# Kernel tuning notes

Hardware: AMD Instinct MI355X
Metric: run time of the kernel (lower is better)

The kernel has to match this reference:

```python
import jax, jax.numpy as jnp
import numpy as np

# Module config (init_kwargs): shape_data=(5,32,32), pow=1, diff_only=False
N_T, N_Y, N_X = 5, 32, 32
N = N_Y * N_X          # nb_nodes = 1024
N_B = 2                # batch
DX = DY = DT = 1.0


def softplus_b(x, beta):
    # torch F.softplus(x, beta) = (1/beta) * log(1 + exp(beta*x))
    return jax.nn.softplus(beta * x) / beta


def build_A(kappa, m, H):
    """Dense finite-difference SPDE operator A = kappa^2 I + m.grad - div(H grad).
    kappa: (N,), m: (2,N), H: (2,2,N). Returns (N,N).
    (DiffOperator source is not in the provided snippet; this is the standard
    4dvarnet SPDE 9-point stencil discretization with dx=dy=1.)"""
    idx = jnp.arange(N)
    xx = idx % N_X
    yy = idx // N_X
    H11, H22 = H[0, 0], H[1, 1]
    H12 = 0.5 * (H[0, 1] + H[1, 0])
    m1, m2 = m[0], m[1]
    center = kappa ** 2 + 2.0 * H11 + 2.0 * H22
    A = jnp.zeros((N, N), dtype=kappa.dtype).at[idx, idx].set(center)
    stencil = [
        ( 1,  0, -H11 + 0.5 * m1),
        (-1,  0, -H11 - 0.5 * m1),
        ( 0,  1, -H22 + 0.5 * m2),
        ( 0, -1, -H22 - 0.5 * m2),
        ( 1,  1, -0.5 * H12),
        (-1, -1, -0.5 * H12),
        ( 1, -1,  0.5 * H12),
        (-1,  1,  0.5 * H12),
    ]
    for dxo, dyo, c in stencil:
        nx_, ny_ = xx + dxo, yy + dyo
        valid = (nx_ >= 0) & (nx_ < N_X) & (ny_ >= 0) & (ny_ < N_Y)
        nbr = jnp.clip(ny_, 0, N_Y - 1) * N_X + jnp.clip(nx_, 0, N_X - 1)
        A = A.at[idx, nbr].add(jnp.where(valid, c, 0.0))
    return A


def decode_params(params):
    """Faithful decode_param_CNN.forward (including its raw-reshape axis mixing)."""
    nb = params.shape[0]
    kappa = softplus_b(params[:, :N_T], 10.0)
    kappa = kappa.reshape(nb, 1, N, N_T)                     # raw reshape as in torch
    m = jnp.stack([params[:, N_T:2 * N_T], params[:, 2 * N_T:3 * N_T]], axis=1)
    m = m.reshape(nb, 2, N, N_T)                             # raw reshape as in torch
    gamma = softplus_b(params[:, 3 * N_T:4 * N_T], 10.0)
    gamma = gamma.transpose(0, 2, 3, 1).reshape(nb, N * N_T)  # (y,x,t) order
    vx = params[:, 4 * N_T:5 * N_T].transpose(0, 2, 3, 1).reshape(nb, N * N_T)
    vy = params[:, 5 * N_T:6 * N_T].transpose(0, 2, 3, 1).reshape(nb, N * N_T)
    vxy = jnp.stack([vx, vy], axis=2)                        # (b, K, 2)
    # H[b,i,j,k] = gamma[b,k]*delta_ij + v_i[b,k]*v_j[b,k]
    H = (jnp.eye(2, dtype=params.dtype)[None, :, :, None] * gamma[:, None, None, :]
         + jnp.einsum('bki,bkj->bijk', vxy, vxy))
    H = H.reshape(nb, 2, 2, N, N_T)
    return kappa, m, H


def reference(params):
    """Prior_SPDE.forward(decode_param_CNN(params), square_root=False) -> dense Q.
    Note: in create_Q (diff_only=False) tau is overwritten with ones and
    QR/Q0 are reassigned to Id / B0^T B0, so tau channels are dead code."""
    kappa, m, H = decode_params(params)
    # operators built for time indices k+1, k=0..n_t-2
    kap_t = jnp.moveaxis(kappa[:, 0, :, 1:], -1, 1).reshape(N_B * (N_T - 1), N)
    m_t = jnp.moveaxis(m[:, :, :, 1:], -1, 1).reshape(N_B * (N_T - 1), 2, N)
    H_t = jnp.moveaxis(H[:, :, :, :, 1:], -1, 1).reshape(N_B * (N_T - 1), 2, 2, N)
    A = jax.vmap(build_A)(kap_t, m_t, H_t).reshape(N_B, N_T - 1, N, N)
    I = jnp.eye(N, dtype=params.dtype)
    invM = A * DT + I                      # Id + dt*B, B = A (pow=1)
    M2 = jnp.matmul(invM, invM)            # inv_M[i]^2
    B0 = A[:, 0]
    Q = jnp.zeros((N_B, N_T * N, N_T * N), dtype=params.dtype)
    s = lambda i: slice(i * N, (i + 1) * N)
    # row 0: [B0^T B0 + I, -inv_M[0], 0...]
    Q = Q.at[:, s(0), s(0)].set(jnp.einsum('bki,bkj->bij', B0, B0) + I)
    Q = Q.at[:, s(0), s(1)].set(-invM[:, 0])
    # rows 1..n_t-2: [..., -inv_M[i-1], inv_M[i-1]^2 + I, -inv_M[i], ...]
    for i in range(1, N_T - 1):
        Q = Q.at[:, s(i), s(i - 1)].set(-invM[:, i - 1])
        Q = Q.at[:, s(i), s(i)].set(M2[:, i - 1] + I)
        Q = Q.at[:, s(i), s(i + 1)].set(-invM[:, i])
    # last row: [..., -inv_M[n_t-2], inv_M[n_t-2]^2]
    Q = Q.at[:, s(N_T - 1), s(N_T - 2)].set(-invM[:, N_T - 2])
    Q = Q.at[:, s(N_T - 1), s(N_T - 1)].set(M2[:, N_T - 2])
    Q = 0.5 * (Q + jnp.swapaxes(Q, 1, 2)) + 0.05 * jnp.eye(N_T * N, dtype=params.dtype)
    return Q


def setup_inputs() -> dict:
    key = jax.random.key(0)
    params = jax.random.normal(key, (N_B, 7 * N_T, N_Y, N_X), dtype=jnp.float32)
    return {"params": params}
```

## Files before the change

kernel.cpp:

```cpp
#include <hip/hip_runtime.h>


#define AC_OFF   0
#define OFFD_OFF 73728
#define DIAG_OFF 147456

__device__ __forceinline__ float softplus10(float x) {
  float z = 10.f * x;
  return (fmaxf(z, 0.f) + log1pf(expf(-fabsf(z)))) * 0.1f;
}

__global__ __launch_bounds__(256) void decode_kernel(
    const float* __restrict__ P0, float* __restrict__ Ac) {
  int gid = blockIdx.x * 256 + threadIdx.x;
  if (gid >= 8 * 1024) return;
  int i = gid >> 10;
  int p = gid & 1023;
  int b = i >> 2;
  int t = (i & 3) + 1;
  const float* P = P0 + b * 35 * 1024;

  int qq = p * 5 + t;
  int c  = qq >> 10;
  int r  = qq & 1023;
  float kap = softplus10(P[(0 + c) * 1024 + r]);
  float m1  = P[(5 + c) * 1024 + r];
  float m2  = P[(10 + c) * 1024 + r];

  float g  = softplus10(P[(15 + t) * 1024 + p]);
  float vx = P[(20 + t) * 1024 + p];
  float vy = P[(25 + t) * 1024 + p];

  float H11 = g + vx * vx;
  float H22 = g + vy * vy;
  float H12 = vx * vy;

  float co[9];
  co[4] = kap * kap + 2.f * H11 + 2.f * H22;
  co[5] = -H11 + 0.5f * m1;
  co[3] = -H11 - 0.5f * m1;
  co[7] = -H22 + 0.5f * m2;
  co[1] = -H22 - 0.5f * m2;
  co[8] = -0.5f * H12;
  co[0] = -0.5f * H12;
  co[2] =  0.5f * H12;
  co[6] =  0.5f * H12;

  int px = p & 31, py = p >> 5;
  #pragma unroll
  for (int o = 0; o < 9; o++) {
    const int dx = o % 3 - 1, dy = o / 3 - 1;
    int nx = px + dx, ny = py + dy;
    bool valid = (nx >= 0) & (nx < 32) & (ny >= 0) & (ny < 32);
    Ac[(i * 1024 + p) * 9 + o] = (o == 4) ? co[4] : (valid ? co[o] : 0.f);
  }
}

__device__ __forceinline__ float m2e(const float* __restrict__ Ac, int i, int p, int q) {
  int px = p & 31, py = p >> 5, qx = q & 31, qy = q >> 5;
  float s = 0.f;
  #pragma unroll
  for (int o = 0; o < 9; o++) {
    const int dx = o % 3 - 1, dy = o / 3 - 1;
    int kx = px + dx, ky = py + dy;
    if (kx < 0 || kx > 31 || ky < 0 || ky > 31) continue;
    int k = ky * 32 + kx;
    float a = Ac[(i * 1024 + p) * 9 + o] + (o == 4 ? 1.f : 0.f);
    int ddx = qx - kx, ddy = qy - ky;
    if (ddx < -1 || ddx > 1 || ddy < -1 || ddy > 1) continue;
    float bb = Ac[(i * 1024 + k) * 9 + (ddy + 1) * 3 + (ddx + 1)] + (k == q ? 1.f : 0.f);
    s += a * bb;
  }
  return s;
}

__device__ __forceinline__ float btb(const float* __restrict__ Ac, int i0, int p, int q) {
  int px = p & 31, py = p >> 5, qx = q & 31, qy = q >> 5;
  float s = 0.f;
  #pragma unroll
  for (int o = 0; o < 9; o++) {
    const int dx = o % 3 - 1, dy = o / 3 - 1;
    int kx = px + dx, ky = py + dy;
    if (kx < 0 || kx > 31 || ky < 0 || ky > 31) continue;
    int k = ky * 32 + kx;
    float bkp = Ac[(i0 * 1024 + k) * 9 + (8 - o)];
    int ddx = qx - kx, ddy = qy - ky;
    if (ddx < -1 || ddx > 1 || ddy < -1 || ddy > 1) continue;
    float bkq = Ac[(i0 * 1024 + k) * 9 + (ddy + 1) * 3 + (ddx + 1)];
    s += bkp * bkq;
  }
  return s;
}

__global__ __launch_bounds__(256) void tables_kernel(float* __restrict__ ws) {
  const float* Ac = ws + AC_OFF;
  int gid = blockIdx.x * 256 + threadIdx.x;
  if (gid < 73728) {
    int i = gid / 9216;
    int rem = gid - i * 9216;
    int p = rem / 9;
    int o = rem - p * 9;
    int px = p & 31, py = p >> 5;
    int dx = o % 3 - 1, dy = o / 3 - 1;
    float v = 0.f;
    if (o == 4) {
      v = -(Ac[(i * 1024 + p) * 9 + 4] + 1.f);
    } else {
      int nx = px + dx, ny = py + dy;
      if (nx >= 0 && nx < 32 && ny >= 0 && ny < 32) {
        int q = ny * 32 + nx;
        v = -0.5f * (Ac[(i * 1024 + p) * 9 + o] + Ac[(i * 1024 + q) * 9 + (8 - o)]);
      }
    }
    ws[OFFD_OFF + gid] = v;
  } else {
    int e = gid - 73728;
    if (e >= 256000) return;
    int j = e / 25600;
    int rem = e - j * 25600;
    int p = rem / 25;
    int w = rem - p * 25;
    int b = j / 5, rb = j - b * 5;
    int px = p & 31, py = p >> 5;
    int dx = w % 5 - 2, dy = w / 5 - 2;
    int nx = px + dx, ny = py + dy;
    float v = 0.f;
    if (nx >= 0 && nx < 32 && ny >= 0 && ny < 32) {
      int q = ny * 32 + nx;
      if (rb == 0) {
        v = btb(Ac, b * 4, p, q) + (p == q ? 1.05f : 0.f);
      } else {
        int i = b * 4 + rb - 1;
        float diagAdd = (rb <= 3 ? 1.05f : 0.05f);
        v = 0.5f * (m2e(Ac, i, p, q) + m2e(Ac, i, q, p)) + (p == q ? diagAdd : 0.f);
      }
    }
    ws[DIAG_OFF + e] = v;
  }
}

__global__ __launch_bounds__(256) void fill_kernel(
    const float* __restrict__ ws, float4* __restrict__ out) {
  const int cb  = blockIdx.x;
  const int row = blockIdx.y;
  const int b   = blockIdx.z;
  const int tx  = threadIdx.x;
  const int rb  = row >> 10;
  const int p   = row & 1023;
  const int d   = cb - rb;
  const long oidx = (long)b * 6553600 + (long)row * 1280 + cb * 256 + tx;

  float4 v = make_float4(0.f, 0.f, 0.f, 0.f);
  if (d >= -1 && d <= 1) {
    const int q0  = tx * 4;
    const int qy  = q0 >> 5;
    const int qx0 = q0 & 31;
    const int px  = p & 31, py = p >> 5;
    const int dy  = qy - py;
    float rr[4] = {0.f, 0.f, 0.f, 0.f};
    if (d != 0) {
      if (dy >= -1 && dy <= 1) {
        const int i = b * 4 + (d > 0 ? rb : cb);
        const float* t = ws + OFFD_OFF + ((i * 1024 + p) * 9 + (dy + 1) * 3 + 1) - px;
        #pragma unroll
        for (int jj = 0; jj < 4; jj++) {
          int dx = qx0 + jj - px;
          if (dx >= -1 && dx <= 1) rr[jj] = t[qx0 + jj];
        }
      }
    } else {
      if (dy >= -2 && dy <= 2) {
        const int j = b * 5 + rb;
        const float* t = ws + DIAG_OFF + ((j * 1024 + p) * 25 + (dy + 2) * 5 + 2) - px;
        #pragma unroll
        for (int jj = 0; jj < 4; jj++) {
          int dx = qx0 + jj - px;
          if (dx >= -2 && dx <= 2) rr[jj] = t[qx0 + jj];
        }
      }
    }
    v = make_float4(rr[0], rr[1], rr[2], rr[3]);
  }
  out[oidx] = v;
}

extern "C" void kernel_launch(void* const* d_in, const int* in_sizes, int n_in,
                              void* d_out, int out_size, void* d_ws, size_t ws_size,
                              hipStream_t stream) {
  const float* params = (const float*)d_in[0];
  float* ws = (float*)d_ws;
  float4* out = (float4*)d_out;

  decode_kernel<<<32, 256, 0, stream>>>(params, ws + AC_OFF);
  tables_kernel<<<1288, 256, 0, stream>>>(ws);
  dim3 grid(5, 5120, 2);
  fill_kernel<<<grid, 256, 0, stream>>>(ws, out);
}
```

Before: 208.9 us.

## Split dense fill into nontemporal zero pass plus sparse band scatter

Replaces the fill kernel, which computed every float4 of the 210 MB output with banded branching, with two kernels. A grid-stride zero kernel writes the whole matrix using nontemporal vector stores, and a band kernel then scatters only the nonzero stencil entries (25 diagonal-block and 9 off-diagonal-block values per row). The aim is a pure streaming write for the bulk of the output. In exchange it adds a launch, scattered scalar writes, and an ordering dependency between the two passes on the same stream.

Measured after the change: 236.9 us. 1.13x slower.

```diff
diff --git a/kernel.cpp b/kernel.cpp
--- a/kernel.cpp
+++ b/kernel.cpp
@@ -4,6 +4,8 @@
 #define AC_OFF   0
 #define OFFD_OFF 73728
 #define DIAG_OFF 147456
+
+typedef float vfloat4 __attribute__((ext_vector_type(4)));
 
 __device__ __forceinline__ float softplus10(float x) {
   float z = 10.f * x;
@@ -139,49 +141,55 @@
   }
 }
 
-__global__ __launch_bounds__(256) void fill_kernel(
-    const float* __restrict__ ws, float4* __restrict__ out) {
-  const int cb  = blockIdx.x;
-  const int row = blockIdx.y;
-  const int b   = blockIdx.z;
-  const int tx  = threadIdx.x;
+__global__ __launch_bounds__(256) void zero_kernel(float* __restrict__ out) {
+  const long n4 = 13107200;
+  long idx = (long)blockIdx.x * 256 + threadIdx.x;
+  const long stride = (long)gridDim.x * 256;
+  vfloat4* o4 = (vfloat4*)out;
+  const vfloat4 z = (vfloat4)(0.f);
+  for (; idx < n4; idx += stride) {
+    __builtin_nontemporal_store(z, &o4[idx]);
+  }
+}
+
+__global__ __launch_bounds__(256) void band_kernel(
+    const float* __restrict__ ws, float* __restrict__ out) {
+  const int row = blockIdx.x * 4 + (threadIdx.x >> 6);
+  const int b   = blockIdx.y;
+  const int t   = threadIdx.x & 63;
   const int rb  = row >> 10;
   const int p   = row & 1023;
-  const int d   = cb - rb;
-  const long oidx = (long)b * 6553600 + (long)row * 1280 + cb * 256 + tx;
-
-  float4 v = make_float4(0.f, 0.f, 0.f, 0.f);
-  if (d >= -1 && d <= 1) {
-    const int q0  = tx * 4;
-    const int qy  = q0 >> 5;
-    const int qx0 = q0 & 31;
-    const int px  = p & 31, py = p >> 5;
-    const int dy  = qy - py;
-    float rr[4] = {0.f, 0.f, 0.f, 0.f};
-    if (d != 0) {
-      if (dy >= -1 && dy <= 1) {
-        const int i = b * 4 + (d > 0 ? rb : cb);
-        const float* t = ws + OFFD_OFF + ((i * 1024 + p) * 9 + (dy + 1) * 3 + 1) - px;
-        #pragma unroll
-        for (int jj = 0; jj < 4; jj++) {
-          int dx = qx0 + jj - px;
-          if (dx >= -1 && dx <= 1) rr[jj] = t[qx0 + jj];
-        }
-      }
-    } else {
-      if (dy >= -2 && dy <= 2) {
-        const int j = b * 5 + rb;
-        const float* t = ws + DIAG_OFF + ((j * 1024 + p) * 25 + (dy + 2) * 5 + 2) - px;
-        #pragma unroll
-        for (int jj = 0; jj < 4; jj++) {
-          int dx = qx0 + jj - px;
-          if (dx >= -2 && dx <= 2) rr[jj] = t[qx0 + jj];
-        }
-      }
-    }
-    v = make_float4(rr[0], rr[1], rr[2], rr[3]);
-  }
-  out[oidx] = v;
+  const int px  = p & 31, py = p >> 5;
+
+  int cb, dx, dy;
+  float v;
+  if (t < 25) {
+    cb = rb;
+    dx = t % 5 - 2;
+    dy = t / 5 - 2;
+    v = ws[DIAG_OFF + ((b * 5 + rb) * 1024 + p) * 25 + t];
+  } else if (t < 34) {
+    if (rb == 0) return;
+    cb = rb - 1;
+    const int o = t - 25;
+    dx = o % 3 - 1;
+    dy = o / 3 - 1;
+    v = ws[OFFD_OFF + ((b * 4 + rb - 1) * 1024 + p) * 9 + o];
+  } else if (t < 43) {
+    if (rb == 4) return;
+    cb = rb + 1;
+    const int o = t - 34;
+    dx = o % 3 - 1;
+    dy = o / 3 - 1;
+    v = ws[OFFD_OFF + ((b * 4 + rb) * 1024 + p) * 9 + o];
+  } else {
+    return;
+  }
+
+  const int nx = px + dx, ny = py + dy;
+  if (nx < 0 || nx > 31 || ny < 0 || ny > 31) return;
+  const int q = ny * 32 + nx;
+  out[(long)b * 26214400 + (long)row * 5120 + cb * 1024 + q] = v;
 }
 
 extern "C" void kernel_launch(void* const* d_in, const int* in_sizes, int n_in,
@@ -189,10 +197,11 @@
                               hipStream_t stream) {
   const float* params = (const float*)d_in[0];
   float* ws = (float*)d_ws;
-  float4* out = (float4*)d_out;
+  float* out = (float*)d_out;
 
   decode_kernel<<<32, 256, 0, stream>>>(params, ws + AC_OFF);
   tables_kernel<<<1288, 256, 0, stream>>>(ws);
-  dim3 grid(5, 5120, 2);
-  fill_kernel<<<grid, 256, 0, stream>>>(ws, out);
-}
+  zero_kernel<<<6400, 256, 0, stream>>>(out);
+  dim3 bgrid(1280, 2);
+  band_kernel<<<bgrid, 256, 0, stream>>>(ws, out);
+}
```

## Fuse decode into table kernel via LDS and write full rows per block

Applied to the files above, without the earlier changes.

Folds the stencil-coefficient decode into the table-building kernel. Each block recomputes the 1024-node coefficient set into shared memory and builds its slice of the off-diagonal and diagonal stencil tables from LDS, which removes one launch and the global round trip for the coefficients. The fill kernel now has one block per output row that writes all five column blocks, so each block loads its stencil values once instead of once per column block. In exchange the decode work is repeated across 16 slices per table, and the fused kernel runs on only 160 blocks.

Measured after the change: 215.7 us. 1.03x slower.

```diff
diff --git a/kernel.cpp b/kernel.cpp
--- a/kernel.cpp
+++ b/kernel.cpp
@@ -1,62 +1,17 @@
 #include <hip/hip_runtime.h>
 
 
-#define AC_OFF   0
 #define OFFD_OFF 73728
 #define DIAG_OFF 147456
+
+typedef float vfloat4 __attribute__((ext_vector_type(4)));
 
 __device__ __forceinline__ float softplus10(float x) {
   float z = 10.f * x;
   return (fmaxf(z, 0.f) + log1pf(expf(-fabsf(z)))) * 0.1f;
 }
 
-__global__ __launch_bounds__(256) void decode_kernel(
-    const float* __restrict__ P0, float* __restrict__ Ac) {
-  int gid = blockIdx.x * 256 + threadIdx.x;
-  if (gid >= 8 * 1024) return;
-  int i = gid >> 10;
-  int p = gid & 1023;
-  int b = i >> 2;
-  int t = (i & 3) + 1;
-  const float* P = P0 + b * 35 * 1024;
-
-  int qq = p * 5 + t;
-  int c  = qq >> 10;
-  int r  = qq & 1023;
-  float kap = softplus10(P[(0 + c) * 1024 + r]);
-  float m1  = P[(5 + c) * 1024 + r];
-  float m2  = P[(10 + c) * 1024 + r];
-
-  float g  = softplus10(P[(15 + t) * 1024 + p]);
-  float vx = P[(20 + t) * 1024 + p];
-  float vy = P[(25 + t) * 1024 + p];
-
-  float H11 = g + vx * vx;
-  float H22 = g + vy * vy;
-  float H12 = vx * vy;
-
-  float co[9];
-  co[4] = kap * kap + 2.f * H11 + 2.f * H22;
-  co[5] = -H11 + 0.5f * m1;
-  co[3] = -H11 - 0.5f * m1;
-  co[7] = -H22 + 0.5f * m2;
-  co[1] = -H22 - 0.5f * m2;
-  co[8] = -0.5f * H12;
-  co[0] = -0.5f * H12;
-  co[2] =  0.5f * H12;
-  co[6] =  0.5f * H12;
-
-  int px = p & 31, py = p >> 5;
-  #pragma unroll
-  for (int o = 0; o < 9; o++) {
-    const int dx = o % 3 - 1, dy = o / 3 - 1;
-    int nx = px + dx, ny = py + dy;
-    bool valid = (nx >= 0) & (nx < 32) & (ny >= 0) & (ny < 32);
-    Ac[(i * 1024 + p) * 9 + o] = (o == 4) ? co[4] : (valid ? co[o] : 0.f);
-  }
-}
-
-__device__ __forceinline__ float m2e(const float* __restrict__ Ac, int i, int p, int q) {
+__device__ __forceinline__ float m2e_lds(const float* ac, int p, int q) {
   int px = p & 31, py = p >> 5, qx = q & 31, qy = q >> 5;
   float s = 0.f;
   #pragma unroll
@@ -65,16 +20,16 @@
     int kx = px + dx, ky = py + dy;
     if (kx < 0 || kx > 31 || ky < 0 || ky > 31) continue;
     int k = ky * 32 + kx;
-    float a = Ac[(i * 1024 + p) * 9 + o] + (o == 4 ? 1.f : 0.f);
+    float a = ac[p * 9 + o] + (o == 4 ? 1.f : 0.f);
     int ddx = qx - kx, ddy = qy - ky;
     if (ddx < -1 || ddx > 1 || ddy < -1 || ddy > 1) continue;
-    float bb = Ac[(i * 1024 + k) * 9 + (ddy + 1) * 3 + (ddx + 1)] + (k == q ? 1.f : 0.f);
+    float bb = ac[k * 9 + (ddy + 1) * 3 + (ddx + 1)] + (k == q ? 1.f : 0.f);
     s += a * bb;
   }
   return s;
 }
 
-__device__ __forceinline__ float btb(const float* __restrict__ Ac, int i0, int p, int q) {
+__device__ __forceinline__ float btb_lds(const float* ac, int p, int q) {
   int px = p & 31, py = p >> 5, qx = q & 31, qy = q >> 5;
   float s = 0.f;
   #pragma unroll
@@ -83,44 +38,87 @@
     int kx = px + dx, ky = py + dy;
     if (kx < 0 || kx > 31 || ky < 0 || ky > 31) continue;
     int k = ky * 32 + kx;
-    float bkp = Ac[(i0 * 1024 + k) * 9 + (8 - o)];
+    float bkp = ac[k * 9 + (8 - o)];
     int ddx = qx - kx, ddy = qy - ky;
     if (ddx < -1 || ddx > 1 || ddy < -1 || ddy > 1) continue;
-    float bkq = Ac[(i0 * 1024 + k) * 9 + (ddy + 1) * 3 + (ddx + 1)];
+    float bkq = ac[k * 9 + (ddy + 1) * 3 + (ddx + 1)];
     s += bkp * bkq;
   }
   return s;
 }
 
-__global__ __launch_bounds__(256) void tables_kernel(float* __restrict__ ws) {
-  const float* Ac = ws + AC_OFF;
-  int gid = blockIdx.x * 256 + threadIdx.x;
-  if (gid < 73728) {
-    int i = gid / 9216;
-    int rem = gid - i * 9216;
-    int p = rem / 9;
-    int o = rem - p * 9;
+__global__ __launch_bounds__(256) void tables_fused(
+    const float* __restrict__ P0, float* __restrict__ ws) {
+  __shared__ float ac[9216];
+  const int j  = blockIdx.x;
+  const int sl = blockIdx.y;
+  const int b  = j / 5, rb = j - b * 5;
+  const int i_ac = b * 4 + (rb == 0 ? 0 : rb - 1);
+  const int tt = (i_ac & 3) + 1;
+  const float* P = P0 + b * 35 * 1024;
+  const int t = threadIdx.x;
+
+  #pragma unroll
+  for (int k = 0; k < 4; k++) {
+    int p = t + k * 256;
+    int qq = p * 5 + tt;
+    int c  = qq >> 10;
+    int r  = qq & 1023;
+    float kap = softplus10(P[(0 + c) * 1024 + r]);
+    float m1  = P[(5 + c) * 1024 + r];
+    float m2  = P[(10 + c) * 1024 + r];
+    float g  = softplus10(P[(15 + tt) * 1024 + p]);
+    float vx = P[(20 + tt) * 1024 + p];
+    float vy = P[(25 + tt) * 1024 + p];
+    float H11 = g + vx * vx;
+    float H22 = g + vy * vy;
+    float H12 = vx * vy;
+    float co[9];
+    co[4] = kap * kap + 2.f * H11 + 2.f * H22;
+    co[5] = -H11 + 0.5f * m1;
+    co[3] = -H11 - 0.5f * m1;
+    co[7] = -H22 + 0.5f * m2;
+    co[1] = -H22 - 0.5f * m2;
+    co[8] = -0.5f * H12;
+    co[0] = -0.5f * H12;
+    co[2] =  0.5f * H12;
+    co[6] =  0.5f * H12;
     int px = p & 31, py = p >> 5;
-    int dx = o % 3 - 1, dy = o / 3 - 1;
-    float v = 0.f;
-    if (o == 4) {
-      v = -(Ac[(i * 1024 + p) * 9 + 4] + 1.f);
-    } else {
+    #pragma unroll
+    for (int o = 0; o < 9; o++) {
+      const int dx = o % 3 - 1, dy = o / 3 - 1;
       int nx = px + dx, ny = py + dy;
-      if (nx >= 0 && nx < 32 && ny >= 0 && ny < 32) {
-        int q = ny * 32 + nx;
-        v = -0.5f * (Ac[(i * 1024 + p) * 9 + o] + Ac[(i * 1024 + q) * 9 + (8 - o)]);
-      }
-    }
-    ws[OFFD_OFF + gid] = v;
-  } else {
-    int e = gid - 73728;
-    if (e >= 256000) return;
-    int j = e / 25600;
-    int rem = e - j * 25600;
-    int p = rem / 25;
-    int w = rem - p * 25;
-    int b = j / 5, rb = j - b * 5;
+      bool valid = (nx >= 0) & (nx < 32) & (ny >= 0) & (ny < 32);
+      ac[p * 9 + o] = (o == 4) ? co[4] : (valid ? co[o] : 0.f);
+    }
+  }
+  __syncthreads();
+
+  if (rb >= 1) {
+    for (int e = t; e < 576; e += 256) {
+      int pl = e / 9;
+      int o  = e - pl * 9;
+      int p  = sl * 64 + pl;
+      int px = p & 31, py = p >> 5;
+      float v = 0.f;
+      if (o == 4) {
+        v = -(ac[p * 9 + 4] + 1.f);
+      } else {
+        int dx = o % 3 - 1, dy = o / 3 - 1;
+        int nx = px + dx, ny = py + dy;
+        if (nx >= 0 && nx < 32 && ny >= 0 && ny < 32) {
+          int q = ny * 32 + nx;
+          v = -0.5f * (ac[p * 9 + o] + ac[q * 9 + (8 - o)]);
+        }
+      }
+      ws[OFFD_OFF + (i_ac * 1024 + p) * 9 + o] = v;
+    }
+  }
+
+  for (int e = t; e < 1600; e += 256) {
+    int pl = e / 25;
+    int w  = e - pl * 25;
+    int p  = sl * 64 + pl;
     int px = p & 31, py = p >> 5;
     int dx = w % 5 - 2, dy = w / 5 - 2;
     int nx = px + dx, ny = py + dy;
@@ -128,60 +126,77 @@
     if (nx >= 0 && nx < 32 && ny >= 0 && ny < 32) {
       int q = ny * 32 + nx;
       if (rb == 0) {
-        v = btb(Ac, b * 4, p, q) + (p == q ? 1.05f : 0.f);
+        v = btb_lds(ac, p, q) + (p == q ? 1.05f : 0.f);
       } else {
-        int i = b * 4 + rb - 1;
         float diagAdd = (rb <= 3 ? 1.05f : 0.05f);
-        v = 0.5f * (m2e(Ac, i, p, q) + m2e(Ac, i, q, p)) + (p == q ? diagAdd : 0.f);
-      }
-    }
-    ws[DIAG_OFF + e] = v;
-  }
-}
-
-__global__ __launch_bounds__(256) void fill_kernel(
-    const float* __restrict__ ws, float4* __restrict__ out) {
-  const int cb  = blockIdx.x;
-  const int row = blockIdx.y;
-  const int b   = blockIdx.z;
-  const int tx  = threadIdx.x;
+        v = 0.5f * (m2e_lds(ac, p, q) + m2e_lds(ac, q, p)) + (p == q ? diagAdd : 0.f);
+      }
+    }
+    ws[DIAG_OFF + (j * 1024 + p) * 25 + w] = v;
+  }
+}
+
+__global__ __launch_bounds__(256) void fill2(
+    const float* __restrict__ ws, float* __restrict__ out) {
+  const int row = blockIdx.x;
+  const int b   = blockIdx.y;
+  const int t   = threadIdx.x;
   const int rb  = row >> 10;
   const int p   = row & 1023;
-  const int d   = cb - rb;
-  const long oidx = (long)b * 6553600 + (long)row * 1280 + cb * 256 + tx;
-
-  float4 v = make_float4(0.f, 0.f, 0.f, 0.f);
-  if (d >= -1 && d <= 1) {
-    const int q0  = tx * 4;
-    const int qy  = q0 >> 5;
-    const int qx0 = q0 & 31;
-    const int px  = p & 31, py = p >> 5;
-    const int dy  = qy - py;
-    float rr[4] = {0.f, 0.f, 0.f, 0.f};
-    if (d != 0) {
-      if (dy >= -1 && dy <= 1) {
-        const int i = b * 4 + (d > 0 ? rb : cb);
-        const float* t = ws + OFFD_OFF + ((i * 1024 + p) * 9 + (dy + 1) * 3 + 1) - px;
-        #pragma unroll
-        for (int jj = 0; jj < 4; jj++) {
-          int dx = qx0 + jj - px;
-          if (dx >= -1 && dx <= 1) rr[jj] = t[qx0 + jj];
-        }
-      }
-    } else {
-      if (dy >= -2 && dy <= 2) {
-        const int j = b * 5 + rb;
-        const float* t = ws + DIAG_OFF + ((j * 1024 + p) * 25 + (dy + 2) * 5 + 2) - px;
-        #pragma unroll
-        for (int jj = 0; jj < 4; jj++) {
-          int dx = qx0 + jj - px;
-          if (dx >= -2 && dx <= 2) rr[jj] = t[qx0 + jj];
-        }
-      }
-    }
-    v = make_float4(rr[0], rr[1], rr[2], rr[3]);
-  }
-  out[oidx] = v;
+  const int px  = p & 31, py = p >> 5;
+  const int q0  = t * 4;
+  const int qy  = q0 >> 5;
+  const int qx0 = q0 & 31;
+  const int dy  = qy - py;
+
+  float dv[4] = {0.f, 0.f, 0.f, 0.f};
+  float lv[4] = {0.f, 0.f, 0.f, 0.f};
+  float rv[4] = {0.f, 0.f, 0.f, 0.f};
+
+  if (dy >= -2 && dy <= 2) {
+    const float* tp = ws + DIAG_OFF +
+        (((b * 5 + rb) * 1024 + p) * 25 + (dy + 2) * 5 + 2) - px;
+    #pragma unroll
+    for (int jj = 0; jj < 4; jj++) {
+      int dx = qx0 + jj - px;
+      if (dx >= -2 && dx <= 2) dv[jj] = tp[qx0 + jj];
+    }
+  }
+  if (dy >= -1 && dy <= 1) {
+    if (rb >= 1) {
+      const float* tp = ws + OFFD_OFF +
+          (((b * 4 + rb - 1) * 1024 + p) * 9 + (dy + 1) * 3 + 1) - px;
+      #pragma unroll
+      for (int jj = 0; jj < 4; jj++) {
+        int dx = qx0 + jj - px;
+        if (dx >= -1 && dx <= 1) lv[jj] = tp[qx0 + jj];
+      }
+    }
+    if (rb <= 3) {
+      const float* tp = ws + OFFD_OFF +
+          (((b * 4 + rb) * 1024 + p) * 9 + (dy + 1) * 3 + 1) - px;
+      #pragma unroll
+      for (int jj = 0; jj < 4; jj++) {
+        int dx = qx0 + jj - px;
+        if (dx >= -1 && dx <= 1) rv[jj] = tp[qx0 + jj];
+      }
+    }
+  }
+
+  vfloat4* o4 = (vfloat4*)out;
+  const long base = (long)b * 6553600 + (long)row * 1280 + t;
+  #pragma unroll
+  for (int cb = 0; cb < 5; cb++) {
+    vfloat4 v = (vfloat4)(0.f);
+    if (cb == rb) {
+      v[0] = dv[0]; v[1] = dv[1]; v[2] = dv[2]; v[3] = dv[3];
+    } else if (cb == rb - 1) {
+      v[0] = lv[0]; v[1] = lv[1]; v[2] = lv[2]; v[3] = lv[3];
+    } else if (cb == rb + 1) {
+      v[0] = rv[0]; v[1] = rv[1]; v[2] = rv[2]; v[3] = rv[3];
+    }
+    o4[base + cb * 256] = v;
+  }
 }
 
 extern "C" void kernel_launch(void* const* d_in, const int* in_sizes, int n_in,
@@ -189,10 +204,10 @@
                               hipStream_t stream) {
   const float* params = (const float*)d_in[0];
   float* ws = (float*)d_ws;
-  float4* out = (float4*)d_out;
-
-  decode_kernel<<<32, 256, 0, stream>>>(params, ws + AC_OFF);
-  tables_kernel<<<1288, 256, 0, stream>>>(ws);
-  dim3 grid(5, 5120, 2);
-  fill_kernel<<<grid, 256, 0, stream>>>(ws, out);
-}
+  float* out = (float*)d_out;
+
+  dim3 g1(10, 16);
+  tables_fused<<<g1, 256, 0, stream>>>(params, ws);
+  dim3 g2(5120, 2);
+  fill2<<<g2, 256, 0, stream>>>(ws, out);
+}
```
